# Optimization experiments

Hardware: AMD Instinct MI355X
Metric: run time of the kernel (lower is better)

## Reference

```python
import jax, jax.numpy as jnp
import numpy as np

POI, EMB, UNITS, QDIM, B = 5000, 256, 512, 256, 64


def setup_inputs() -> dict:
    key = jax.random.key(0)
    ks = jax.random.split(key, 16)
    s = 0.05
    return {
        "x": jax.random.randint(ks[0], (B,), 0, POI),
        "query": jax.random.normal(ks[1], (B, QDIM), jnp.float32),
        "poi_embedding": jax.random.normal(ks[2], (POI, EMB), jnp.float32),
        "A_hat": jax.random.normal(ks[3], (B, B), jnp.float32),
        "dec_hidden": jax.random.normal(ks[4], (B, UNITS), jnp.float32),
        "cat_dec_hidden": jax.random.normal(ks[5], (1, B, UNITS), jnp.float32),
        # GRUCell params (keras order z, r, h; reset_after=True -> bias [2, 3*units])
        "gru_kernel": jax.random.normal(ks[6], (EMB + QDIM, 3 * UNITS), jnp.float32) * s,
        "gru_rec_kernel": jax.random.normal(ks[7], (UNITS, 3 * UNITS), jnp.float32) * s,
        "gru_bias": jax.random.normal(ks[8], (2, 3 * UNITS), jnp.float32) * s,
        # Bahdanau attention params
        "W1_w": jax.random.normal(ks[9], (EMB, UNITS), jnp.float32) * s,
        "W1_b": jnp.zeros((UNITS,), jnp.float32),
        "W2_w": jax.random.normal(ks[10], (UNITS, UNITS), jnp.float32) * s,
        "W2_b": jnp.zeros((UNITS,), jnp.float32),
        "V_w": jax.random.normal(ks[11], (UNITS, 1), jnp.float32) * s,
        "V_b": jnp.zeros((1,), jnp.float32),
        # output dense: concat(context EMB, output_ UNITS, cat_hidden UNITS) -> POI
        "fc_w": jax.random.normal(ks[12], (EMB + 2 * UNITS, POI), jnp.float32) * s,
        "fc_b": jnp.zeros((POI,), jnp.float32),
    }


def _gru_cell(x, h, kernel, rec_kernel, bias):
    # keras GRUCell, reset_after=True, gate order (z, r, h)
    xm = x @ kernel + bias[0]        # [B, 3U]
    hm = h @ rec_kernel + bias[1]    # [B, 3U]
    xz, xr, xh = jnp.split(xm, 3, axis=-1)
    hz, hr, hh = jnp.split(hm, 3, axis=-1)
    z = jax.nn.sigmoid(xz + hz)
    r = jax.nn.sigmoid(xr + hr)
    h_cand = jnp.tanh(xh + r * hh)
    h_new = z * h + (1.0 - z) * h_cand
    return h_new, h_new


def reference(x, query, poi_embedding, A_hat, dec_hidden, cat_dec_hidden,
              gru_kernel, gru_rec_kernel, gru_bias,
              W1_w, W1_b, W2_w, W2_b, V_w, V_b, fc_w, fc_b):
    emb = poi_embedding
    x1 = jnp.concatenate([emb[x], query], axis=1)          # [B, EMB+QDIM]
    output_, state = _gru_cell(x1, dec_hidden, gru_kernel, gru_rec_kernel, gru_bias)
    # Bahdanau attention: values are the full embedding table [POI, EMB]
    v_proj = emb @ W1_w + W1_b                              # [POI, U]
    q_proj = output_ @ W2_w + W2_b                          # [B, U]
    score = jnp.tanh(v_proj[None, :, :] + q_proj[:, None, :]) @ V_w + V_b  # [B, POI, 1]
    attn = jax.nn.softmax(score, axis=1)                    # [B, POI, 1]
    context = jnp.sum(attn * emb[None, :, :], axis=1)       # [B, EMB]
    out_cat = jnp.concatenate([context, output_, cat_dec_hidden[0]], axis=1)
    logits = out_cat @ fc_w + fc_b                          # [B, POI]
    return (logits, state, output_)
```

## Files before the change

kernel.cpp:

```cpp
#include <hip/hip_runtime.h>
#include <hip/hip_bf16.h>

typedef __bf16 bf16;
typedef __bf16 bf16x8 __attribute__((ext_vector_type(8)));
typedef float f32x4 __attribute__((ext_vector_type(4)));

#define BB 64
#define EMB 256
#define UNITS 512
#define POI 5000
#define KCAT 1280
#define SCLD 5024
#define L2E 1.4426950408889634f

__device__ __forceinline__ float rcp_(float x){ return __builtin_amdgcn_rcpf(x); }
__device__ __forceinline__ float exp2_(float x){ return __builtin_amdgcn_exp2f(x); }

__device__ __forceinline__ f32x4 mm16f(const float* __restrict__ A, const float* __restrict__ B,
                                       int lda, int ldb, int K, int mr, int nc, int lane){
  int q = lane >> 4;
  f32x4 acc = {0.f,0.f,0.f,0.f};
  const float* ap = A + (size_t)mr*lda + q*8;
  const float* bp = B + (size_t)(q*8)*ldb + nc;
#pragma unroll 2
  for(int k0 = 0; k0 < K; k0 += 32){
    f32x4 a0 = *(const f32x4*)ap;
    f32x4 a1 = *(const f32x4*)(ap+4);
    bf16x8 a, b;
#pragma unroll
    for(int j=0;j<4;j++){ a[j] = (bf16)a0[j]; a[4+j] = (bf16)a1[j]; }
#pragma unroll
    for(int j=0;j<8;j++) b[j] = (bf16)bp[(size_t)j*ldb];
    acc = __builtin_amdgcn_mfma_f32_16x16x32_bf16(a, b, acc, 0, 0, 0);
    ap += 32; bp += (size_t)32*ldb;
  }
  return acc;
}

__global__ void k_prep(const int* __restrict__ x, const float* __restrict__ query,
                       const float* __restrict__ emb, const float* __restrict__ catd,
                       float* __restrict__ x1, float* __restrict__ outc){
  int b = blockIdx.x, t = threadIdx.x;
  int row = x[b];
  x1[b*512 + t]       = emb[(size_t)row*EMB + t];
  x1[b*512 + 256 + t] = query[(size_t)b*256 + t];
  outc[b*KCAT + 768 + t]       = catd[(size_t)b*512 + t];
  outc[b*KCAT + 768 + 256 + t] = catd[(size_t)b*512 + 256 + t];
}

__global__ __launch_bounds__(256) void k_gru(const float* __restrict__ x1, const float* __restrict__ h0,
    const float* __restrict__ gruK, const float* __restrict__ gruR,
    float* __restrict__ xmP, float* __restrict__ hmP){
  int lane = threadIdx.x & 63, w = threadIdx.x >> 6;
  int col = blockIdx.x*16 + (lane & 15);
  const float* A = blockIdx.y ? h0 : x1;
  const float* B = blockIdx.y ? gruR : gruK;
  float* C = (blockIdx.y ? hmP : xmP) + (size_t)blockIdx.z*BB*1536;
  int z = blockIdx.z;
  f32x4 acc = mm16f(A + z*256, B + (size_t)(z*256)*1536, 512, 1536, 256,
                    w*16 + (lane & 15), col, lane);
  int rb = w*16 + (lane >> 4)*4;
#pragma unroll
  for(int r=0;r<4;r++) C[(size_t)(rb+r)*1536 + col] = acc[r];
}

__global__ void k_gates(const float* __restrict__ xmP, const float* __restrict__ hmP,
                        const float* __restrict__ bias, const float* __restrict__ h0,
                        float* __restrict__ hn, float* __restrict__ outc, float* __restrict__ dout){
  int b = blockIdx.x, u = threadIdx.x;
  const float* x0 = xmP + b*1536; const float* x1s = xmP + (size_t)BB*1536 + b*1536;
  const float* h0s = hmP + b*1536; const float* h1s = hmP + (size_t)BB*1536 + b*1536;
  float xz = x0[u]      + x1s[u]      + bias[u];
  float xg = x0[512+u]  + x1s[512+u]  + bias[512+u];
  float xh = x0[1024+u] + x1s[1024+u] + bias[1024+u];
  float hz = h0s[u]      + h1s[u]      + bias[1536+u];
  float hg = h0s[512+u]  + h1s[512+u]  + bias[2048+u];
  float hh = h0s[1024+u] + h1s[1024+u] + bias[2560+u];
  float z = rcp_(1.f + exp2_(-L2E*(xz+hz)));
  float r = rcp_(1.f + exp2_(-L2E*(xg+hg)));
  float ca = xh + r*hh;
  ca = fminf(fmaxf(ca, -15.f), 15.f);
  float e = exp2_(2.f*L2E*ca);
  float hc = (e - 1.f)*rcp_(e + 1.f);
  float h = h0[b*512+u];
  float v = z*h + (1.f - z)*hc;
  hn[b*512+u] = v;
  outc[b*KCAT + 256 + u] = v;
  dout[(size_t)POI*BB + (size_t)b*512 + u] = v;
  dout[(size_t)POI*BB + (size_t)BB*512 + (size_t)b*512 + u] = v;
}

__global__ __launch_bounds__(256) void k_qproj(const float* __restrict__ hn, const float* __restrict__ W2,
                        const float* __restrict__ W2b, float* __restrict__ Eq){
  int lane = threadIdx.x & 63, w = threadIdx.x >> 6;
  int col = blockIdx.x*16 + (lane & 15);
  f32x4 acc = mm16f(hn, W2, UNITS, UNITS, UNITS, w*16 + (lane & 15), col, lane);
  float bn = W2b[col];
  int rb = w*16 + (lane >> 4)*4;
#pragma unroll
  for(int r=0;r<4;r++){
    float v = (acc[r] + bn)*(2.f*L2E);
    Eq[(rb+r)*UNITS + col] = exp2_(fminf(fmaxf(v, -40.f), 40.f));
  }
}

__global__ __launch_bounds__(256) void k_vscore(const float* __restrict__ emb, const float* __restrict__ W1,
    const float* __restrict__ W1b, const float* __restrict__ Eq,
    const float* __restrict__ Vw, float* __restrict__ scS){
  __shared__ float evs[16][132];
  __shared__ float Qs[64][68];
  __shared__ float vws[128];
  int t = threadIdx.x, lane = t & 63, w = t >> 6;
  int p0 = blockIdx.x*16, uh = blockIdx.y*128;
  int mr = p0 + (lane & 15); if(mr > POI-1) mr = POI-1;
#pragma unroll
  for(int i=0;i<2;i++){
    int ncl = (w + i*4)*16 + (lane & 15);
    f32x4 acc = mm16f(emb, W1, EMB, UNITS, EMB, mr, uh + ncl, lane);
    float bn = W1b[uh + ncl];
    int rb = (lane >> 4)*4;
#pragma unroll
    for(int r=0;r<4;r++){
      float v = (acc[r] + bn)*(2.f*L2E);
      evs[rb+r][ncl] = exp2_(fminf(fmaxf(v, -40.f), 40.f));
    }
  }
  if(t < 128) vws[t] = Vw[uh + t];
  int tp = t & 7, tb = t >> 3;
  float s00=0.f, s01=0.f, s10=0.f, s11=0.f;
  for(int c=0;c<2;c++){
    __syncthreads();
    int ub = c*64;
    for(int i=t;i<4096;i+=256){ int b=i>>6, u=i&63; Qs[b][u] = Eq[b*UNITS + uh + ub + u]; }
    __syncthreads();
#pragma unroll
    for(int u4=0;u4<16;u4++){
      f32x4 e0 = *(f32x4*)&evs[2*tp][ub+u4*4];
      f32x4 e1 = *(f32x4*)&evs[2*tp+1][ub+u4*4];
      f32x4 q0 = *(f32x4*)&Qs[2*tb][u4*4];
      f32x4 q1 = *(f32x4*)&Qs[2*tb+1][u4*4];
      f32x4 w4 = *(f32x4*)&vws[ub+u4*4];
#pragma unroll
      for(int e=0;e<4;e++){
        float wv = w4[e];
        s00 += wv * rcp_(e0[e]*q0[e] + 1.f);
        s01 += wv * rcp_(e0[e]*q1[e] + 1.f);
        s10 += wv * rcp_(e1[e]*q0[e] + 1.f);
        s11 += wv * rcp_(e1[e]*q1[e] + 1.f);
      }
    }
  }
  float* s = scS + (size_t)blockIdx.y*BB*SCLD;
  int pA = p0 + 2*tp, bA = 2*tb;
  if(pA < POI)  { s[(size_t)bA*SCLD + pA]   = s00; s[(size_t)(bA+1)*SCLD + pA]   = s01; }
  if(pA+1 < POI){ s[(size_t)bA*SCLD + pA+1] = s10; s[(size_t)(bA+1)*SCLD + pA+1] = s11; }
}

__global__ __launch_bounds__(512) void k_softmax(float* __restrict__ sc, const float* __restrict__ Vw,
                                                 float* __restrict__ outc){
  __shared__ float red[512];
  int b = blockIdx.x, t = threadIdx.x;
  if(t < 256) outc[b*KCAT + t] = 0.f;
  red[t] = Vw[t];
  __syncthreads();
  for(int o=256;o>0;o>>=1){ if(t<o) red[t]+=red[t+o]; __syncthreads(); }
  float SW = red[0]; __syncthreads();
  float* sA = sc + (size_t)b*SCLD;
  const float* s1 = sA + (size_t)BB*SCLD;
  const float* s2 = sA + (size_t)2*BB*SCLD;
  const float* s3 = sA + (size_t)3*BB*SCLD;
  float mx = -3.4e38f;
  for(int p=t;p<POI;p+=512){
    float s = SW - 2.f*(sA[p] + s1[p] + s2[p] + s3[p]);
    sA[p] = s;
    mx = fmaxf(mx, s);
  }
  red[t] = mx; __syncthreads();
  for(int o=256;o>0;o>>=1){ if(t<o) red[t]=fmaxf(red[t],red[t+o]); __syncthreads(); }
  float M = red[0]; __syncthreads();
  float sum = 0.f;
  for(int p=t;p<POI;p+=512){
    float wv = exp2_((sA[p] - M)*L2E);
    sA[p] = wv;
    sum += wv;
  }
  red[t] = sum; __syncthreads();
  for(int o=256;o>0;o>>=1){ if(t<o) red[t]+=red[t+o]; __syncthreads(); }
  float iv = rcp_(red[0]);
  for(int p=t;p<POI;p+=512) sA[p] *= iv;
  if(t < SCLD-POI) sA[POI + t] = 0.f;
}

__global__ __launch_bounds__(256) void k_ctx(const float* __restrict__ wb, const float* __restrict__ emb,
                                             float* __restrict__ outc){
  int lane = threadIdx.x & 63, w = threadIdx.x >> 6;
  int n = blockIdx.x*16 + (lane & 15);
  int ky = blockIdx.y;
  int kbeg = ky*384;
  int mr = w*16 + (lane & 15);
  f32x4 acc = mm16f(wb + kbeg, emb + (size_t)kbeg*EMB, SCLD, EMB, 384, mr, n, lane);
  if(ky == 12){
    int q = lane >> 4;
    const float* ap = wb + (size_t)mr*SCLD + 4992 + q*8;
    bf16x8 a, bfr;
#pragma unroll
    for(int j=0;j<8;j++) a[j] = (bf16)ap[j];
#pragma unroll
    for(int j=0;j<8;j++){
      int k = 4992 + q*8 + j; int kc = k < POI ? k : POI-1;
      bfr[j] = (bf16)emb[(size_t)kc*EMB + n];
    }
    acc = __builtin_amdgcn_mfma_f32_16x16x32_bf16(a, bfr, acc, 0, 0, 0);
  }
  int rb = w*16 + (lane >> 4)*4;
#pragma unroll
  for(int r=0;r<4;r++) atomicAdd(&outc[(size_t)(rb+r)*KCAT + n], acc[r]);
}

__global__ __launch_bounds__(256) void k_logits(const float* __restrict__ A, const float* __restrict__ Bw,
                        const float* __restrict__ fcb, float* __restrict__ out){
  int lane = threadIdx.x & 63, w = threadIdx.x >> 6;
  int n = blockIdx.x*16 + (lane & 15);
  int nc = n < POI ? n : POI-1;
  int ky = blockIdx.y, kbeg = ky*320;
  f32x4 acc = mm16f(A + kbeg, Bw + (size_t)kbeg*POI, KCAT, POI, 320,
                    w*16 + (lane & 15), nc, lane);
  int rb = w*16 + (lane >> 4)*4;
  if(n < POI){
    float bn = (ky == 0) ? fcb[n] : 0.f;
#pragma unroll
    for(int r=0;r<4;r++) atomicAdd(&out[(size_t)(rb+r)*POI + n], acc[r] + bn);
  }
}

extern "C" void kernel_launch(void* const* d_in, const int* in_sizes, int n_in,
                              void* d_out, int out_size, void* d_ws, size_t ws_size,
                              hipStream_t stream){
  const int*   x     = (const int*)d_in[0];
  const float* query = (const float*)d_in[1];
  const float* emb   = (const float*)d_in[2];
  const float* h0    = (const float*)d_in[4];
  const float* catd  = (const float*)d_in[5];
  const float* gruK  = (const float*)d_in[6];
  const float* gruR  = (const float*)d_in[7];
  const float* gruB  = (const float*)d_in[8];
  const float* W1    = (const float*)d_in[9];
  const float* W1b   = (const float*)d_in[10];
  const float* W2    = (const float*)d_in[11];
  const float* W2b   = (const float*)d_in[12];
  const float* Vw    = (const float*)d_in[13];
  const float* fcw   = (const float*)d_in[15];
  const float* fcb   = (const float*)d_in[16];
  float* out = (float*)d_out;

  char* ws = (char*)d_ws;
  size_t off = 0;
  auto alloc = [&](size_t bytes)->void*{ void* p = ws + off; off += (bytes + 255) & ~(size_t)255; return p; };
  float* x1   = (float*)alloc((size_t)BB*512*4);
  float* outc = (float*)alloc((size_t)BB*KCAT*4);
  float* xmP  = (float*)alloc((size_t)2*BB*1536*4);
  float* hmP  = (float*)alloc((size_t)2*BB*1536*4);
  float* hn   = (float*)alloc((size_t)BB*512*4);
  float* Eq   = (float*)alloc((size_t)BB*512*4);
  float* sc   = (float*)alloc((size_t)4*BB*SCLD*4);

  hipMemsetAsync(out, 0, (size_t)BB*POI*sizeof(float), stream);
  k_prep   <<<BB, 256, 0, stream>>>(x, query, emb, catd, x1, outc);
  k_gru    <<<dim3(96,2,2), 256, 0, stream>>>(x1, h0, gruK, gruR, xmP, hmP);
  k_gates  <<<BB, 512, 0, stream>>>(xmP, hmP, gruB, h0, hn, outc, out);
  k_qproj  <<<32, 256, 0, stream>>>(hn, W2, W2b, Eq);
  k_vscore <<<dim3(313,4), 256, 0, stream>>>(emb, W1, W1b, Eq, Vw, sc);
  k_softmax<<<BB, 512, 0, stream>>>(sc, Vw, outc);
  k_ctx    <<<dim3(16,13), 256, 0, stream>>>(sc, emb, outc);
  k_logits <<<dim3(313,4), 256, 0, stream>>>(outc, fcw, fcb, out);
}
```

Baseline: 198.4 us.

## Fuse prep gather into GRU GEMM and split attention scoring over more slabs

Drops the k_prep launch: the GRU GEMM reads embedding rows and query directly through the index, and the cat_dec_hidden copy moves into the gates kernel. The attention scoring kernel is templated on the number of unit slices. When the workspace is large enough it uses 8 slices of 64 units, which doubles the grid, and it reads Eq straight from global memory instead of staging it in shared memory, removing syncs. The softmax sums a variable number of partial slabs. This costs more workspace and more partial-score traffic.

Measured after the change: 207.5 us. 1.05x slower.

```diff
diff --git a/kernel.cpp b/kernel.cpp
--- a/kernel.cpp
+++ b/kernel.cpp
@@ -16,11 +16,11 @@
 __device__ __forceinline__ float rcp_(float x){ return __builtin_amdgcn_rcpf(x); }
 __device__ __forceinline__ float exp2_(float x){ return __builtin_amdgcn_exp2f(x); }
 
-__device__ __forceinline__ f32x4 mm16f(const float* __restrict__ A, const float* __restrict__ B,
-                                       int lda, int ldb, int K, int mr, int nc, int lane){
+__device__ __forceinline__ f32x4 mm16r(const float* __restrict__ ap, const float* __restrict__ B,
+                                       int ldb, int K, int nc, int lane){
   int q = lane >> 4;
   f32x4 acc = {0.f,0.f,0.f,0.f};
-  const float* ap = A + (size_t)mr*lda + q*8;
+  ap += q*8;
   const float* bp = B + (size_t)(q*8)*ldb + nc;
 #pragma unroll 2
   for(int k0 = 0; k0 < K; k0 += 32){
@@ -37,28 +37,32 @@
   return acc;
 }
 
-__global__ void k_prep(const int* __restrict__ x, const float* __restrict__ query,
-                       const float* __restrict__ emb, const float* __restrict__ catd,
-                       float* __restrict__ x1, float* __restrict__ outc){
-  int b = blockIdx.x, t = threadIdx.x;
-  int row = x[b];
-  x1[b*512 + t]       = emb[(size_t)row*EMB + t];
-  x1[b*512 + 256 + t] = query[(size_t)b*256 + t];
-  outc[b*KCAT + 768 + t]       = catd[(size_t)b*512 + t];
-  outc[b*KCAT + 768 + 256 + t] = catd[(size_t)b*512 + 256 + t];
-}
-
-__global__ __launch_bounds__(256) void k_gru(const float* __restrict__ x1, const float* __restrict__ h0,
+__device__ __forceinline__ f32x4 mm16f(const float* __restrict__ A, const float* __restrict__ B,
+                                       int lda, int ldb, int K, int mr, int nc, int lane){
+  return mm16r(A + (size_t)mr*lda, B, ldb, K, nc, lane);
+}
+
+__global__ __launch_bounds__(256) void k_gru(const int* __restrict__ x, const float* __restrict__ query,
+    const float* __restrict__ emb, const float* __restrict__ h0,
     const float* __restrict__ gruK, const float* __restrict__ gruR,
     float* __restrict__ xmP, float* __restrict__ hmP){
   int lane = threadIdx.x & 63, w = threadIdx.x >> 6;
   int col = blockIdx.x*16 + (lane & 15);
-  const float* A = blockIdx.y ? h0 : x1;
-  const float* B = blockIdx.y ? gruR : gruK;
-  float* C = (blockIdx.y ? hmP : xmP) + (size_t)blockIdx.z*BB*1536;
   int z = blockIdx.z;
-  f32x4 acc = mm16f(A + z*256, B + (size_t)(z*256)*1536, 512, 1536, 256,
-                    w*16 + (lane & 15), col, lane);
+  int mr = w*16 + (lane & 15);
+  const float* arow;
+  const float* B;
+  float* C;
+  if(blockIdx.y){
+    arow = h0 + (size_t)mr*512 + z*256;
+    B = gruR + (size_t)(z*256)*1536;
+    C = hmP + (size_t)z*BB*1536;
+  } else {
+    arow = z ? (query + (size_t)mr*256) : (emb + (size_t)x[mr]*EMB);
+    B = gruK + (size_t)(z*256)*1536;
+    C = xmP + (size_t)z*BB*1536;
+  }
+  f32x4 acc = mm16r(arow, B, 1536, 256, col, lane);
   int rb = w*16 + (lane >> 4)*4;
 #pragma unroll
   for(int r=0;r<4;r++) C[(size_t)(rb+r)*1536 + col] = acc[r];
@@ -66,6 +70,7 @@
 
 __global__ void k_gates(const float* __restrict__ xmP, const float* __restrict__ hmP,
                         const float* __restrict__ bias, const float* __restrict__ h0,
+                        const float* __restrict__ catd,
                         float* __restrict__ hn, float* __restrict__ outc, float* __restrict__ dout){
   int b = blockIdx.x, u = threadIdx.x;
   const float* x0 = xmP + b*1536; const float* x1s = xmP + (size_t)BB*1536 + b*1536;
@@ -86,6 +91,7 @@
   float v = z*h + (1.f - z)*hc;
   hn[b*512+u] = v;
   outc[b*KCAT + 256 + u] = v;
+  outc[b*KCAT + 768 + u] = catd[(size_t)b*512 + u];
   dout[(size_t)POI*BB + (size_t)b*512 + u] = v;
   dout[(size_t)POI*BB + (size_t)BB*512 + (size_t)b*512 + u] = v;
 }
@@ -104,17 +110,18 @@
   }
 }
 
-__global__ __launch_bounds__(256) void k_vscore(const float* __restrict__ emb, const float* __restrict__ W1,
+template<int NY>
+__global__ __launch_bounds__(256, 6) void k_vscore(const float* __restrict__ emb, const float* __restrict__ W1,
     const float* __restrict__ W1b, const float* __restrict__ Eq,
     const float* __restrict__ Vw, float* __restrict__ scS){
-  __shared__ float evs[16][132];
-  __shared__ float Qs[64][68];
-  __shared__ float vws[128];
+  constexpr int USL = 512/NY;
+  __shared__ float evs[16][USL+4];
+  __shared__ float vws[USL];
   int t = threadIdx.x, lane = t & 63, w = t >> 6;
-  int p0 = blockIdx.x*16, uh = blockIdx.y*128;
+  int p0 = blockIdx.x*16, uh = blockIdx.y*USL;
   int mr = p0 + (lane & 15); if(mr > POI-1) mr = POI-1;
 #pragma unroll
-  for(int i=0;i<2;i++){
+  for(int i=0;i<USL/64;i++){
     int ncl = (w + i*4)*16 + (lane & 15);
     f32x4 acc = mm16f(emb, W1, EMB, UNITS, EMB, mr, uh + ncl, lane);
     float bn = W1b[uh + ncl];
@@ -125,29 +132,26 @@
       evs[rb+r][ncl] = exp2_(fminf(fmaxf(v, -40.f), 40.f));
     }
   }
-  if(t < 128) vws[t] = Vw[uh + t];
+  if(t < USL) vws[t] = Vw[uh + t];
+  __syncthreads();
   int tp = t & 7, tb = t >> 3;
+  const float* q0p = Eq + (size_t)(2*tb)*UNITS + uh;
+  const float* q1p = q0p + UNITS;
   float s00=0.f, s01=0.f, s10=0.f, s11=0.f;
-  for(int c=0;c<2;c++){
-    __syncthreads();
-    int ub = c*64;
-    for(int i=t;i<4096;i+=256){ int b=i>>6, u=i&63; Qs[b][u] = Eq[b*UNITS + uh + ub + u]; }
-    __syncthreads();
-#pragma unroll
-    for(int u4=0;u4<16;u4++){
-      f32x4 e0 = *(f32x4*)&evs[2*tp][ub+u4*4];
-      f32x4 e1 = *(f32x4*)&evs[2*tp+1][ub+u4*4];
-      f32x4 q0 = *(f32x4*)&Qs[2*tb][u4*4];
-      f32x4 q1 = *(f32x4*)&Qs[2*tb+1][u4*4];
-      f32x4 w4 = *(f32x4*)&vws[ub+u4*4];
-#pragma unroll
-      for(int e=0;e<4;e++){
-        float wv = w4[e];
-        s00 += wv * rcp_(e0[e]*q0[e] + 1.f);
-        s01 += wv * rcp_(e0[e]*q1[e] + 1.f);
-        s10 += wv * rcp_(e1[e]*q0[e] + 1.f);
-        s11 += wv * rcp_(e1[e]*q1[e] + 1.f);
-      }
+#pragma unroll 2
+  for(int u4=0; u4<USL/4; ++u4){
+    f32x4 e0 = *(const f32x4*)&evs[2*tp][4*u4];
+    f32x4 e1 = *(const f32x4*)&evs[2*tp+1][4*u4];
+    f32x4 q0 = *(const f32x4*)&q0p[4*u4];
+    f32x4 q1 = *(const f32x4*)&q1p[4*u4];
+    f32x4 w4 = *(const f32x4*)&vws[4*u4];
+#pragma unroll
+    for(int e=0;e<4;e++){
+      float wv = w4[e];
+      s00 += wv * rcp_(e0[e]*q0[e] + 1.f);
+      s01 += wv * rcp_(e0[e]*q1[e] + 1.f);
+      s10 += wv * rcp_(e1[e]*q0[e] + 1.f);
+      s11 += wv * rcp_(e1[e]*q1[e] + 1.f);
     }
   }
   float* s = scS + (size_t)blockIdx.y*BB*SCLD;
@@ -157,7 +161,7 @@
 }
 
 __global__ __launch_bounds__(512) void k_softmax(float* __restrict__ sc, const float* __restrict__ Vw,
-                                                 float* __restrict__ outc){
+                                                 float* __restrict__ outc, int nslab){
   __shared__ float red[512];
   int b = blockIdx.x, t = threadIdx.x;
   if(t < 256) outc[b*KCAT + t] = 0.f;
@@ -166,12 +170,11 @@
   for(int o=256;o>0;o>>=1){ if(t<o) red[t]+=red[t+o]; __syncthreads(); }
   float SW = red[0]; __syncthreads();
   float* sA = sc + (size_t)b*SCLD;
-  const float* s1 = sA + (size_t)BB*SCLD;
-  const float* s2 = sA + (size_t)2*BB*SCLD;
-  const float* s3 = sA + (size_t)3*BB*SCLD;
   float mx = -3.4e38f;
   for(int p=t;p<POI;p+=512){
-    float s = SW - 2.f*(sA[p] + s1[p] + s2[p] + s3[p]);
+    float acc = sA[p];
+    for(int y=1;y<nslab;y++) acc += sA[(size_t)y*BB*SCLD + p];
+    float s = SW - 2.f*acc;
     sA[p] = s;
     mx = fmaxf(mx, s);
   }
@@ -253,24 +256,27 @@
   const float* fcb   = (const float*)d_in[16];
   float* out = (float*)d_out;
 
+  int nslab = (ws_size >= (size_t)14*1024*1024) ? 8 : 4;
+
   char* ws = (char*)d_ws;
   size_t off = 0;
   auto alloc = [&](size_t bytes)->void*{ void* p = ws + off; off += (bytes + 255) & ~(size_t)255; return p; };
-  float* x1   = (float*)alloc((size_t)BB*512*4);
   float* outc = (float*)alloc((size_t)BB*KCAT*4);
   float* xmP  = (float*)alloc((size_t)2*BB*1536*4);
   float* hmP  = (float*)alloc((size_t)2*BB*1536*4);
   float* hn   = (float*)alloc((size_t)BB*512*4);
   float* Eq   = (float*)alloc((size_t)BB*512*4);
-  float* sc   = (float*)alloc((size_t)4*BB*SCLD*4);
+  float* sc   = (float*)alloc((size_t)nslab*BB*SCLD*4);
 
   hipMemsetAsync(out, 0, (size_t)BB*POI*sizeof(float), stream);
-  k_prep   <<<BB, 256, 0, stream>>>(x, query, emb, catd, x1, outc);
-  k_gru    <<<dim3(96,2,2), 256, 0, stream>>>(x1, h0, gruK, gruR, xmP, hmP);
-  k_gates  <<<BB, 512, 0, stream>>>(xmP, hmP, gruB, h0, hn, outc, out);
+  k_gru    <<<dim3(96,2,2), 256, 0, stream>>>(x, query, emb, h0, gruK, gruR, xmP, hmP);
+  k_gates  <<<BB, 512, 0, stream>>>(xmP, hmP, gruB, h0, catd, hn, outc, out);
   k_qproj  <<<32, 256, 0, stream>>>(hn, W2, W2b, Eq);
-  k_vscore <<<dim3(313,4), 256, 0, stream>>>(emb, W1, W1b, Eq, Vw, sc);
-  k_softmax<<<BB, 512, 0, stream>>>(sc, Vw, outc);
+  if(nslab == 8)
+    k_vscore<8><<<dim3(313,8), 256, 0, stream>>>(emb, W1, W1b, Eq, Vw, sc);
+  else
+    k_vscore<4><<<dim3(313,4), 256, 0, stream>>>(emb, W1, W1b, Eq, Vw, sc);
+  k_softmax<<<BB, 512, 0, stream>>>(sc, Vw, outc, nslab);
   k_ctx    <<<dim3(16,13), 256, 0, stream>>>(sc, emb, outc);
   k_logits <<<dim3(313,4), 256, 0, stream>>>(outc, fcw, fcb, out);
 }
```
